# Kernel tuning notes

Measured on AMD Instinct MI355X. Metric: run time of the kernel, lower is better.

Reference implementation:

```python
import jax, jax.numpy as jnp
import numpy as np

# Module hyperparameters (from init_kwargs)
LEARNING_RATE = 0.01  # not used inside compute_weight_update
TAU_PLUS = 20.0
TAU_MINUS = 20.0
A_PLUS = 0.005
A_MINUS = 0.00525
TARGET_RATE = 0.1
HOMEOSTATIC_RATE = 0.001
TAU_HOMEOSTATIC = 1000.0

B, T, N_PRE, N_POST = 16, 8192, 128, 128


def setup_inputs() -> dict:
    key = jax.random.key(0)
    k1, k2, k3 = jax.random.split(key, 3)
    # Bernoulli spike trains at ~target_rate firing probability
    pre_spikes = (jax.random.uniform(k1, (B, T, N_PRE)) < TARGET_RATE).astype(jnp.float32)
    post_spikes = (jax.random.uniform(k2, (B, T, N_POST)) < TARGET_RATE).astype(jnp.float32)
    weights = jax.random.uniform(k3, (N_PRE, N_POST), dtype=jnp.float32)
    return {"pre_spikes": pre_spikes, "post_spikes": post_spikes, "weights": weights, "dt": 1}


def _temporal_corr(x, kernel, pad):
    """Correlate x [B,T,N] along time with 1-D kernel [L], padding pad=(lo,hi)."""
    b, t, n = x.shape
    xr = jnp.moveaxis(x, 1, 2).reshape(b * n, 1, t)  # [B*N, 1, T]
    k = kernel.reshape(1, 1, -1).astype(x.dtype)
    y = jax.lax.conv_general_dilated(
        xr, k, window_strides=(1,), padding=[pad],
        dimension_numbers=("NCH", "OIH", "NCH"))
    return jnp.moveaxis(y.reshape(b, n, t), 2, 1)  # [B,T,N]


def reference(pre_spikes, post_spikes, weights, dt):
    b, t, n_pre = pre_spikes.shape
    dt = float(dt)

    # Homeostatic rate tracking (first call: avg rates initialized to target_rate)
    alpha = dt / TAU_HOMEOSTATIC
    current_post_rate = post_spikes.mean(axis=(0, 1))
    avg_post_rate = (1.0 - alpha) * TARGET_RATE + alpha * current_post_rate

    # Truncated exponential STDP window: tau in 1..min(int(3*tau)-1, ...) = 1..59
    L = int(TAU_PLUS * 3)  # 60 taps (tau=0 tap zeroed)
    taus = jnp.arange(L, dtype=jnp.float32)
    w_plus = jnp.where(taus > 0, A_PLUS * jnp.exp(-taus * dt / TAU_PLUS), 0.0)
    w_minus = jnp.where(taus > 0, A_MINUS * jnp.exp(-taus * dt / TAU_MINUS), 0.0)

    # LTP: post_filt[t] = sum_{tau>=1} w_plus[tau] * post[t+tau] (future, zero-padded)
    post_filt = _temporal_corr(post_spikes, w_plus, (0, L - 1))
    # LTD: pre_filt[t] = sum_{tau>=1} w_minus[tau] * pre[t-tau] (past, zero-padded)
    pre_filt = _temporal_corr(pre_spikes, w_minus[::-1], (L - 1, 0))

    # sum_t mean_b outer(pre[t], post_filt[t]) - outer(pre_filt[t], post[t]), then /T
    ltp = jnp.einsum("btp,btq->pq", pre_spikes, post_filt)
    ltd = jnp.einsum("btp,btq->pq", pre_filt, post_spikes)
    stdp_update = (ltp - ltd) / (b * t)

    # Homeostatic regulation pulls post rate toward target
    post_rate_error = avg_post_rate - TARGET_RATE
    homeostatic_update = -HOMEOSTATIC_RATE * post_rate_error[None, :] * weights

    return stdp_update + homeostatic_update
```

## Files before the change

kernel.cpp:

```cpp
#include <hip/hip_runtime.h>

#define BB 16
#define TT 8192
#define NN 128
constexpr int CHUNK = 256;
constexpr int NBLK  = BB * TT / CHUNK;
constexpr int OUTN  = NN * NN;
constexpr int GS    = 264;
constexpr int SLOTS = OUTN / 2;
constexpr int KG    = 16;
constexpr int PROWS = 315;

typedef _Float16 f16x8 __attribute__((ext_vector_type(8)));
typedef _Float16 f16x2 __attribute__((ext_vector_type(2)));
typedef float    f32x4 __attribute__((ext_vector_type(4)));

__device__ __forceinline__ unsigned short h16(float x) {
    _Float16 h = (_Float16)x;
    return __builtin_bit_cast(unsigned short, h);
}
__device__ __forceinline__ unsigned int pack2(float x, float y) {
    return (unsigned int)h16(x) | ((unsigned int)h16(y) << 16);
}
__device__ __forceinline__ float2 ldL(const unsigned short* p_lds, int m, int q0) {
    const unsigned int v = *(const unsigned int*)&p_lds[m * NN + q0];
    const f16x2 h = __builtin_bit_cast(f16x2, v);
    return make_float2((float)h[0], (float)h[1]);
}

template<bool ATOMIC>
__global__ __launch_bounds__(512, 4)
void stdp_main(const float* __restrict__ pre, const float* __restrict__ post,
               const int* __restrict__ dtp,
               unsigned int* __restrict__ part, float* __restrict__ wpost,
               float* __restrict__ outat)
{
    __shared__ __align__(16) char smem[PROWS * NN * 2];
    unsigned short* post_lds = (unsigned short*)smem;
    unsigned short* g_lds    = (unsigned short*)smem;
    float*          lds_ps   = (float*)(smem + NN * GS * 2);

    const int tid   = threadIdx.x;
    const int blk   = blockIdx.x;
    const int b     = blk >> 5;
    const int chunk = blk & 31;
    const int t0    = chunk * CHUNK;
    const int wv    = tid >> 6;
    const int lane  = tid & 63;

    const float dtf = (float)(*dtp);
    const float r   = expf(-dtf * (1.0f / 20.0f));

    const float* pb = post + (size_t)b * TT * NN;
    const float* ab = pre  + (size_t)b * TT * NN;

    {
        const int c  = tid & 31;
        const int mr = tid >> 5;
        for (int m = mr; m < PROWS; m += 16) {
            const int t = t0 + 1 + m;
            float4 v = make_float4(0.f, 0.f, 0.f, 0.f);
            if (t < TT) v = *(const float4*)(pb + (size_t)t * NN + c * 4);
            *(uint2*)&post_lds[m * NN + c * 4] = make_uint2(pack2(v.x, v.y), pack2(v.z, v.w));
        }
    }
    __syncthreads();

    const int win  = wv;
    const int q0   = lane * 2;
    const int base = win * 32;
    float ps0 = 0.f, ps1 = 0.f;

    unsigned int pk0[16], pk1[16];
    {
        float2 p  = ldL(post_lds, base + 31, q0);
        float wt  = r;
        float gx = r * p.x, gy = r * p.y;
        ps0 += p.x; ps1 += p.y;
        #pragma unroll
        for (int tau = 2; tau <= 59; ++tau) {
            wt *= r;
            p = ldL(post_lds, base + 30 + tau, q0);
            gx = fmaf(wt, p.x, gx);
            gy = fmaf(wt, p.y, gy);
        }
        const float r60 = wt * r;
        pk0[15] = (unsigned int)h16(gx) << 16;
        pk1[15] = (unsigned int)h16(gy) << 16;
        #pragma unroll
        for (int c = 30; c >= 0; --c) {
            const float2 p1  = ldL(post_lds, base + c,      q0);
            const float2 p60 = ldL(post_lds, base + c + 59, q0);
            gx = r * (gx + p1.x) - r60 * p60.x;
            gy = r * (gy + p1.y) - r60 * p60.y;
            ps0 += p1.x; ps1 += p1.y;
            if (c & 1) {
                pk0[c >> 1] = (unsigned int)h16(gx) << 16;
                pk1[c >> 1] = (unsigned int)h16(gy) << 16;
            } else {
                pk0[c >> 1] |= h16(gx);
                pk1[c >> 1] |= h16(gy);
            }
        }
    }
    __syncthreads();

    {
        unsigned short* d0 = &g_lds[q0 * GS + win * 32];
        unsigned short* d1 = &g_lds[(q0 + 1) * GS + win * 32];
        #pragma unroll
        for (int s = 0; s < 4; ++s) {
            *(uint4*)(d0 + 8 * s) = make_uint4(pk0[4*s], pk0[4*s+1], pk0[4*s+2], pk0[4*s+3]);
            *(uint4*)(d1 + 8 * s) = make_uint4(pk1[4*s], pk1[4*s+1], pk1[4*s+2], pk1[4*s+3]);
        }
        lds_ps[win * NN + q0]     = ps0;
        lds_ps[win * NN + q0 + 1] = ps1;
    }
    __syncthreads();

    const int pr0 = wv * 16;
    f32x4 acc[8];
    #pragma unroll
    for (int qt = 0; qt < 8; ++qt) acc[qt] = (f32x4){0.f, 0.f, 0.f, 0.f};

    for (int ks = 0; ks < 8; ++ks) {
        const int trow = t0 + ks * 32 + (lane >> 4) * 8;
        const float* src = ab + (size_t)trow * NN + pr0 + (lane & 15);
        f16x8 af;
        #pragma unroll
        for (int j = 0; j < 8; ++j)
            af[j] = (_Float16)src[(size_t)j * NN];
        const int koff = ks * 32 + (lane >> 4) * 8;
        #pragma unroll
        for (int qt = 0; qt < 8; ++qt) {
            const f16x8 bf = *(const f16x8*)&g_lds[(qt * 16 + (lane & 15)) * GS + koff];
            acc[qt] = __builtin_amdgcn_mfma_f32_16x16x32_f16(af, bf, acc[qt], 0, 0, 0);
        }
    }

    if constexpr (!ATOMIC) {
        unsigned int* dst = part + ((size_t)blk * 8 + wv) * 1024 + lane;
        #pragma unroll
        for (int qt = 0; qt < 8; ++qt)
            #pragma unroll
            for (int rp = 0; rp < 2; ++rp)
                dst[qt * 128 + rp * 64] = pack2(acc[qt][2 * rp], acc[qt][2 * rp + 1]);
    } else {
        #pragma unroll
        for (int qt = 0; qt < 8; ++qt)
            #pragma unroll
            for (int rg = 0; rg < 4; ++rg) {
                const int prow = pr0 + (lane >> 4) * 4 + rg;
                const int qcol = qt * 16 + (lane & 15);
                atomicAdd(&outat[prow * NN + qcol], acc[qt][rg]);
            }
    }

    __syncthreads();
    if (tid < NN) {
        float s = 0.f;
        #pragma unroll
        for (int w = 0; w < 8; ++w) s += lds_ps[w * NN + tid];
        if (chunk == 0) s += pb[tid];
        if constexpr (ATOMIC) atomicAdd(&wpost[tid], s);
        else wpost[(size_t)tid * NBLK + blk] = s;
    }
}

__global__ void hfac_kernel(const float* __restrict__ wpost, const int* __restrict__ dtp,
                            float* __restrict__ hfac, int nb)
{
    const int q = blockIdx.x;
    float s = 0.f;
    for (int k = threadIdx.x; k < nb; k += 64) s += wpost[(size_t)q * nb + k];
    #pragma unroll
    for (int off = 32; off; off >>= 1) s += __shfl_down(s, off, 64);
    if (threadIdx.x == 0) {
        const float dtf   = (float)(*dtp);
        const float alpha = dtf * 1e-3f;
        const float mean  = s * (1.0f / (float)(BB * TT));
        hfac[q] = -0.001f * (alpha * (mean - 0.1f));
    }
}

__global__ __launch_bounds__(256)
void reduce1(const unsigned int* __restrict__ part, float2* __restrict__ partial2)
{
    const int i  = (blockIdx.x & 31) * 256 + threadIdx.x;
    const int kg = blockIdx.x >> 5;
    float sx = 0.f, sy = 0.f;
    #pragma unroll 8
    for (int k = kg * 32; k < kg * 32 + 32; ++k) {
        const unsigned int v = part[(size_t)k * SLOTS + i];
        const f16x2 h = __builtin_bit_cast(f16x2, v);
        sx += (float)h[0];
        sy += (float)h[1];
    }
    partial2[(size_t)kg * SLOTS + i] = make_float2(sx, sy);
}

__global__ void reduce2(const float2* __restrict__ partial2, const float* __restrict__ hfac,
                        const float* __restrict__ W, float* __restrict__ out)
{
    const int sid = blockIdx.x * 256 + threadIdx.x;
    float sx = 0.f, sy = 0.f;
    #pragma unroll
    for (int r = 0; r < KG; ++r) {
        const float2 v = partial2[(size_t)r * SLOTS + sid];
        sx += v.x; sy += v.y;
    }
    const int lane = sid & 63;
    const int rp   = (sid >> 6) & 1;
    const int qt   = (sid >> 7) & 7;
    const int wv   = sid >> 10;
    const int p    = wv * 16 + ((lane >> 4) << 2) + rp * 2;
    const int q    = qt * 16 + (lane & 15);
    const float scale = (float)((0.005 - 0.00525) / (double)(BB * TT));
    const float hf = hfac[q];
    out[p * NN + q]       = fmaf(sx, scale, hf * W[p * NN + q]);
    out[(p + 1) * NN + q] = fmaf(sy, scale, hf * W[(p + 1) * NN + q]);
}

__global__ void finalize_at(const float* __restrict__ hfac, const float* __restrict__ W,
                            float* __restrict__ out)
{
    const int i = (blockIdx.x * 256 + threadIdx.x) * 2;
    const int q = i & 127;
    const float scale = (float)((0.005 - 0.00525) / (double)(BB * TT));
    float2 s = *(const float2*)(out + i);
    float2 w = *(const float2*)(W + i);
    float2 o;
    o.x = fmaf(s.x, scale, hfac[q] * w.x);
    o.y = fmaf(s.y, scale, hfac[q + 1] * w.y);
    *(float2*)(out + i) = o;
}

extern "C" void kernel_launch(void* const* d_in, const int* in_sizes, int n_in,
                              void* d_out, int out_size, void* d_ws, size_t ws_size,
                              hipStream_t stream)
{
    const float* pre  = (const float*)d_in[0];
    const float* post = (const float*)d_in[1];
    const float* W    = (const float*)d_in[2];
    const int*   dtp  = (const int*)d_in[3];
    float* out = (float*)d_out;

    const size_t part_bytes  = (size_t)NBLK * SLOTS * sizeof(unsigned int);
    const size_t p2_bytes    = (size_t)KG * SLOTS * sizeof(float2);
    const size_t wpost_bytes = (size_t)NBLK * NN * sizeof(float);
    const size_t need = part_bytes + p2_bytes + wpost_bytes + NN * sizeof(float);

    if (ws_size >= need) {
        unsigned int* part = (unsigned int*)d_ws;
        float2* partial2   = (float2*)((char*)d_ws + part_bytes);
        float* wpost       = (float*)((char*)d_ws + part_bytes + p2_bytes);
        float* hfac        = (float*)((char*)d_ws + part_bytes + p2_bytes + wpost_bytes);
        hipLaunchKernelGGL((stdp_main<false>), dim3(NBLK), dim3(512), 0, stream,
                           pre, post, dtp, part, wpost, (float*)nullptr);
        hipLaunchKernelGGL(hfac_kernel, dim3(NN), dim3(64), 0, stream, wpost, dtp, hfac, NBLK);
        hipLaunchKernelGGL(reduce1, dim3(512), dim3(256), 0, stream, part, partial2);
        hipLaunchKernelGGL(reduce2, dim3(SLOTS / 256), dim3(256), 0, stream, partial2, hfac, W, out);
    } else {
        float* wpost = (float*)d_ws;
        float* hfac  = wpost + NN;
        hipMemsetAsync(d_out, 0, OUTN * sizeof(float), stream);
        hipMemsetAsync(wpost, 0, NN * sizeof(float), stream);
        hipLaunchKernelGGL((stdp_main<true>), dim3(NBLK), dim3(512), 0, stream,
                           pre, post, dtp, (unsigned int*)nullptr, wpost, out);
        hipLaunchKernelGGL(hfac_kernel, dim3(NN), dim3(64), 0, stream, wpost, dtp, hfac, 1);
        hipLaunchKernelGGL(finalize_at, dim3(OUTN / 512), dim3(256), 0, stream, hfac, W, out);
    }
}
```

Measured before the change: 172.6 us.

## Fuse two-pass partial reduction into one kernel and prefetch A operand rows

Replaces the reduce1/reduce2 pair with a single finalize_ws kernel. Each block of 512 threads covers 64 output slots, sums the fp16 partials over 8 groups of 64 block-rows, and combines them through shared memory before applying the scale and homeostatic term. This removes one launch and the float2 intermediate buffer round trip, but uses fewer blocks (128) with longer serial loops per thread. The main kernel's MFMA loop is also unrolled and loads the next k-step's A values into registers before issuing the current MFMAs, hiding global load latency at the cost of more registers. Some redundant dead arithmetic is left in the finalize kernel.

After: 164.7 us. 1.05x faster.

```diff
diff --git a/kernel.cpp b/kernel.cpp
--- a/kernel.cpp
+++ b/kernel.cpp
@@ -8,7 +8,6 @@
 constexpr int OUTN  = NN * NN;
 constexpr int GS    = 264;
 constexpr int SLOTS = OUTN / 2;
-constexpr int KG    = 16;
 constexpr int PROWS = 315;
 
 typedef _Float16 f16x8 __attribute__((ext_vector_type(8)));
@@ -123,13 +122,21 @@
     #pragma unroll
     for (int qt = 0; qt < 8; ++qt) acc[qt] = (f32x4){0.f, 0.f, 0.f, 0.f};
 
+    const float* abase = ab + (size_t)(t0 + (lane >> 4) * 8) * NN + pr0 + (lane & 15);
+    float an[8];
+    #pragma unroll
+    for (int j = 0; j < 8; ++j) an[j] = abase[(size_t)j * NN];
+
+    #pragma unroll
     for (int ks = 0; ks < 8; ++ks) {
-        const int trow = t0 + ks * 32 + (lane >> 4) * 8;
-        const float* src = ab + (size_t)trow * NN + pr0 + (lane & 15);
         f16x8 af;
         #pragma unroll
-        for (int j = 0; j < 8; ++j)
-            af[j] = (_Float16)src[(size_t)j * NN];
+        for (int j = 0; j < 8; ++j) af[j] = (_Float16)an[j];
+        if (ks < 7) {
+            const float* src = abase + (size_t)((ks + 1) * 32) * NN;
+            #pragma unroll
+            for (int j = 0; j < 8; ++j) an[j] = src[(size_t)j * NN];
+        }
         const int koff = ks * 32 + (lane >> 4) * 8;
         #pragma unroll
         for (int qt = 0; qt < 8; ++qt) {
@@ -183,42 +190,50 @@
     }
 }
 
-__global__ __launch_bounds__(256)
-void reduce1(const unsigned int* __restrict__ part, float2* __restrict__ partial2)
-{
-    const int i  = (blockIdx.x & 31) * 256 + threadIdx.x;
-    const int kg = blockIdx.x >> 5;
+__global__ __launch_bounds__(512)
+void finalize_ws(const unsigned int* __restrict__ part, const float* __restrict__ hfac,
+                 const float* __restrict__ W, float* __restrict__ out)
+{
+    __shared__ float2 red[512];
+    const int s    = threadIdx.x & 63;
+    const int kq   = threadIdx.x >> 6;
+    const int slot = blockIdx.x * 64 + s;
     float sx = 0.f, sy = 0.f;
     #pragma unroll 8
-    for (int k = kg * 32; k < kg * 32 + 32; ++k) {
-        const unsigned int v = part[(size_t)k * SLOTS + i];
+    for (int k = kq * 64; k < kq * 64 + 64; ++k) {
+        const unsigned int v = part[(size_t)k * SLOTS + slot];
         const f16x2 h = __builtin_bit_cast(f16x2, v);
         sx += (float)h[0];
         sy += (float)h[1];
     }
-    partial2[(size_t)kg * SLOTS + i] = make_float2(sx, sy);
-}
-
-__global__ void reduce2(const float2* __restrict__ partial2, const float* __restrict__ hfac,
-                        const float* __restrict__ W, float* __restrict__ out)
-{
-    const int sid = blockIdx.x * 256 + threadIdx.x;
-    float sx = 0.f, sy = 0.f;
-    #pragma unroll
-    for (int r = 0; r < KG; ++r) {
-        const float2 v = partial2[(size_t)r * SLOTS + sid];
-        sx += v.x; sy += v.y;
-    }
-    const int lane = sid & 63;
-    const int rp   = (sid >> 6) & 1;
-    const int qt   = (sid >> 7) & 7;
-    const int wv   = sid >> 10;
-    const int p    = wv * 16 + ((lane >> 4) << 2) + rp * 2;
-    const int q    = qt * 16 + (lane & 15);
-    const float scale = (float)((0.005 - 0.00525) / (double)(BB * TT));
-    const float hf = hfac[q];
-    out[p * NN + q]       = fmaf(sx, scale, hf * W[p * NN + q]);
-    out[(p + 1) * NN + q] = fmaf(sy, scale, hf * W[(p + 1) * NN + q]);
+    red[threadIdx.x] = make_float2(sx, sy);
+    __syncthreads();
+    if (threadIdx.x < 64) {
+        #pragma unroll
+        for (int g = 1; g < 8; ++g) {
+            const float2 v = red[g * 64 + s];
+            sx += v.x; sy += v.y;
+        }
+        sx += red[s].x - red[s].x + 0.f;
+        float rx = red[s].x, ry = red[s].y;
+        sx = sx - (sx - sx);
+        float tx = rx, ty = ry;
+        #pragma unroll
+        for (int g = 1; g < 8; ++g) {
+            const float2 v = red[g * 64 + s];
+            tx += v.x; ty += v.y;
+        }
+        const int lane = slot & 63;
+        const int rp   = (slot >> 6) & 1;
+        const int qt   = (slot >> 7) & 7;
+        const int wv   = slot >> 10;
+        const int p    = wv * 16 + ((lane >> 4) << 2) + rp * 2;
+        const int q    = qt * 16 + (lane & 15);
+        const float scale = (float)((0.005 - 0.00525) / (double)(BB * TT));
+        const float hf = hfac[q];
+        out[p * NN + q]       = fmaf(tx, scale, hf * W[p * NN + q]);
+        out[(p + 1) * NN + q] = fmaf(ty, scale, hf * W[(p + 1) * NN + q]);
+    }
 }
 
 __global__ void finalize_at(const float* __restrict__ hfac, const float* __restrict__ W,
@@ -246,20 +261,17 @@
     float* out = (float*)d_out;
 
     const size_t part_bytes  = (size_t)NBLK * SLOTS * sizeof(unsigned int);
-    const size_t p2_bytes    = (size_t)KG * SLOTS * sizeof(float2);
     const size_t wpost_bytes = (size_t)NBLK * NN * sizeof(float);
-    const size_t need = part_bytes + p2_bytes + wpost_bytes + NN * sizeof(float);
+    const size_t need = part_bytes + wpost_bytes + NN * sizeof(float);
 
     if (ws_size >= need) {
         unsigned int* part = (unsigned int*)d_ws;
-        float2* partial2   = (float2*)((char*)d_ws + part_bytes);
-        float* wpost       = (float*)((char*)d_ws + part_bytes + p2_bytes);
-        float* hfac        = (float*)((char*)d_ws + part_bytes + p2_bytes + wpost_bytes);
+        float* wpost       = (float*)((char*)d_ws + part_bytes);
+        float* hfac        = (float*)((char*)d_ws + part_bytes + wpost_bytes);
         hipLaunchKernelGGL((stdp_main<false>), dim3(NBLK), dim3(512), 0, stream,
                            pre, post, dtp, part, wpost, (float*)nullptr);
         hipLaunchKernelGGL(hfac_kernel, dim3(NN), dim3(64), 0, stream, wpost, dtp, hfac, NBLK);
-        hipLaunchKernelGGL(reduce1, dim3(512), dim3(256), 0, stream, part, partial2);
-        hipLaunchKernelGGL(reduce2, dim3(SLOTS / 256), dim3(256), 0, stream, partial2, hfac, W, out);
+        hipLaunchKernelGGL(finalize_ws, dim3(SLOTS / 64), dim3(512), 0, stream, part, hfac, W, out);
     } else {
         float* wpost = (float*)d_ws;
         float* hfac  = wpost + NN;
```
